# Optimization experiments

Measured on AMD Instinct MI355X. Metric: run time of the kernel, lower is better.

The kernel has to match this reference:

```python
import jax, jax.numpy as jnp
import numpy as np

FEATURE_DIM = 1024
HEADS = 16
HEAD_DIM = FEATURE_DIM // HEADS


def setup_inputs() -> dict:
    key = jax.random.key(0)
    ks = jax.random.split(key, 9)
    B, C, T = 4, FEATURE_DIM, 4096
    s = 1.0 / np.sqrt(C)
    inp = {
        "x": jax.random.normal(ks[0], (B, C, T), dtype=jnp.float32),
        "Wq": jax.random.uniform(ks[1], (C, C), jnp.float32, -s, s),
        "bq": jax.random.uniform(ks[2], (C,), jnp.float32, -s, s),
        "Wk": jax.random.uniform(ks[3], (C, C), jnp.float32, -s, s),
        "bk": jax.random.uniform(ks[4], (C,), jnp.float32, -s, s),
        "Wv": jax.random.uniform(ks[5], (C, C), jnp.float32, -s, s),
        "bv": jax.random.uniform(ks[6], (C,), jnp.float32, -s, s),
        "Wo": jax.random.uniform(ks[7], (C, C), jnp.float32, -s, s),
        "bo": jax.random.uniform(ks[8], (C,), jnp.float32, -s, s),
    }
    return inp


def reference(x, Wq, bq, Wk, bk, Wv, bv, Wo, bo):
    B, C, T = x.shape
    H, D = HEADS, HEAD_DIM
    xt = jnp.transpose(x, (0, 2, 1))  # [B, T, C]
    # torch Linear: y = x @ W.T + b
    q = jax.nn.elu(xt @ Wq.T + bq).reshape(B, T, H, D) + 1.0
    k = jax.nn.elu(xt @ Wk.T + bk).reshape(B, T, H, D) + 1.0
    v = (xt @ Wv.T + bv).reshape(B, T, H, D)
    kv = jnp.einsum('bthd,bthe->bhde', k, v)      # [B, H, D, D]
    z = jnp.einsum('bthd,bhd->bth', q, k.sum(axis=1))  # [B, T, H]
    num = jnp.einsum('bthd,bhde->bthe', q, kv)    # [B, T, H, D]
    out = num / (z[..., None] + 1e-6)
    out = out.reshape(B, T, C)
    out = out @ Wo.T + bo  # dropout is identity in eval mode
    return jnp.transpose(out + xt, (0, 2, 1))  # [B, C, T]
```

## Files before the change

kernel.cpp:

```cpp
#include <hip/hip_runtime.h>
#include <hip/hip_bf16.h>
#include <cmath>

typedef unsigned short u16;
typedef unsigned int   u32;

#define BB 4
#define CC 1024
#define TT 4096
#define HH 16
#define DD 64

using bf16x8 = __attribute__((ext_vector_type(8))) __bf16;
using f32x4  = __attribute__((ext_vector_type(4))) float;

union FragU { bf16x8 v; u16 u[8]; };

__device__ __forceinline__ float bf2f(u16 u) {
    union { u32 i; float f; } v; v.i = ((u32)u) << 16; return v.f;
}
__device__ __forceinline__ u16 f2bf(float f) {
    union { float f; u32 i; } v; v.f = f;
    u32 x = v.i;
    return (u16)((x + 0x7fffu + ((x >> 16) & 1u)) >> 16);
}

__device__ __forceinline__ void gl_lds16(const u16* g, u16* l) {
    __builtin_amdgcn_global_load_lds(
        (const __attribute__((address_space(1))) void*)g,
        (__attribute__((address_space(3))) void*)l, 16, 0, 0);
}

__global__ __launch_bounds__(256) void cvt_kernel(
    const float* __restrict__ src, u16* __restrict__ dst, int n)
{
    const int i = (blockIdx.x * 256 + threadIdx.x) * 4;
    if (i < n) {
        const float4 v = *reinterpret_cast<const float4*>(src + i);
        ushort4 o;
        o.x = f2bf(v.x); o.y = f2bf(v.y); o.z = f2bf(v.z); o.w = f2bf(v.w);
        *reinterpret_cast<ushort4*>(dst + i) = o;
    }
}

__global__ __launch_bounds__(256) void transpose_kernel(
    const float* __restrict__ x, u16* __restrict__ xt)
{
    __shared__ u16 tile[64 * 258];
    const int b  = blockIdx.z;
    const int t0 = blockIdx.x * 64;
    const int c0 = blockIdx.y * 256;
    const float* xb  = x  + (size_t)b * CC * TT;
    u16*         xtb = xt + (size_t)b * TT * CC;

    const int tcol = threadIdx.x & 63;
    const int rw   = threadIdx.x >> 6;
    #pragma unroll 8
    for (int p = 0; p < 64; ++p) {
        const int cr = p * 4 + rw;
        tile[tcol * 258 + cr] = f2bf(xb[(size_t)(c0 + cr) * TT + t0 + tcol]);
    }
    __syncthreads();
    const int cp = threadIdx.x & 127;
    const int th = threadIdx.x >> 7;
    #pragma unroll 8
    for (int q = 0; q < 32; ++q) {
        const int tr = q * 2 + th;
        const u32 v = *reinterpret_cast<const u32*>(&tile[tr * 258 + cp * 2]);
        *reinterpret_cast<u32*>(&xtb[(size_t)(t0 + tr) * CC + c0 + cp * 2]) = v;
    }
}

template <int MODE>
__global__ __launch_bounds__(256, 2) void gemm_kernel(
    const u16* __restrict__ A, const u16* __restrict__ W,
    const float* __restrict__ b0, const float* __restrict__ b1,
    const float* __restrict__ b2, u16* __restrict__ Ybf,
    float* __restrict__ Yf, const float* __restrict__ xres,
    int M, int N, int K)
{
    __shared__ char smem[34048];
    u16* As = (u16*)smem;
    u16* Ws = (u16*)(smem + 16384);

    const int tid  = threadIdx.x;
    const int w    = tid >> 6;
    const int lane = tid & 63;
    const int wm = w >> 1, wn = w & 1;
    const int quad = lane >> 4, l16 = lane & 15;
    const int m0 = blockIdx.y * 128;
    const int n0 = blockIdx.x * 128;

    const int srow = lane >> 3;
    const int scol = ((lane & 7) ^ srow) * 8;

    f32x4 acc[4][4];
    #pragma unroll
    for (int i = 0; i < 4; ++i)
        #pragma unroll
        for (int j = 0; j < 4; ++j) acc[i][j] = (f32x4)0.0f;

    for (int k0 = 0; k0 < K; k0 += 64) {
        __syncthreads();
        #pragma unroll
        for (int s = 0; s < 4; ++s)
            gl_lds16(A + (size_t)(m0 + 32 * w + 8 * s + srow) * K + k0 + scol,
                     &As[(32 * w + 8 * s) * 64]);
        #pragma unroll
        for (int s = 0; s < 4; ++s)
            gl_lds16(W + (size_t)(n0 + 32 * w + 8 * s + srow) * K + k0 + scol,
                     &Ws[(32 * w + 8 * s) * 64]);
        __syncthreads();

        #pragma unroll
        for (int sub = 0; sub < 2; ++sub) {
            const int pg = (((sub << 2) | quad) ^ (l16 & 7)) * 8;
            bf16x8 af[4], bfr[4];
            #pragma unroll
            for (int i = 0; i < 4; ++i) {
                af[i]  = *reinterpret_cast<const bf16x8*>(&As[(wm * 64 + i * 16 + l16) * 64 + pg]);
                bfr[i] = *reinterpret_cast<const bf16x8*>(&Ws[(wn * 64 + i * 16 + l16) * 64 + pg]);
            }
            #pragma unroll
            for (int i = 0; i < 4; ++i)
                #pragma unroll
                for (int j = 0; j < 4; ++j)
                    acc[i][j] = __builtin_amdgcn_mfma_f32_16x16x32_bf16(af[i], bfr[j], acc[i][j], 0, 0, 0);
        }
    }

    if (MODE == 2) {
        float* Cs = (float*)smem;
        const int b     = m0 / TT;
        const int tbase = m0 - b * TT;
        const int cl    = lane >> 4;
        #pragma unroll
        for (int hh = 0; hh < 2; ++hh) {
            __syncthreads();
            if (wm == hh) {
                #pragma unroll
                for (int i = 0; i < 4; ++i)
                    #pragma unroll
                    for (int j = 0; j < 4; ++j)
                        #pragma unroll
                        for (int r = 0; r < 4; ++r)
                            Cs[(i * 16 + quad * 4 + r) * 133 + wn * 64 + j * 16 + l16] = acc[i][j][r];
            }
            __syncthreads();
            #pragma unroll
            for (int p = 0; p < 8; ++p) {
                const int col = p * 16 + w * 4 + cl;
                const int tl  = l16 * 4;
                float4 v;
                v.x = Cs[(tl + 0) * 133 + col];
                v.y = Cs[(tl + 1) * 133 + col];
                v.z = Cs[(tl + 2) * 133 + col];
                v.w = Cs[(tl + 3) * 133 + col];
                const float bv = b0[n0 + col];
                const size_t base = ((size_t)b * CC + n0 + col) * TT + tbase + hh * 64 + tl;
                const float4 rx = *reinterpret_cast<const float4*>(&xres[base]);
                v.x += bv + rx.x; v.y += bv + rx.y;
                v.z += bv + rx.z; v.w += bv + rx.w;
                *reinterpret_cast<float4*>(&Yf[base]) = v;
            }
        }
    } else {
        const int seg = n0 >> 10;
        const float* bp = (seg == 0) ? b0 : ((seg == 1) ? b1 : b2);
        u16* Yseg = Ybf + (size_t)seg * M * CC;
        #pragma unroll
        for (int i = 0; i < 4; ++i) {
            const int row = m0 + wm * 64 + i * 16 + quad * 4;
            #pragma unroll
            for (int j = 0; j < 4; ++j) {
                const int colL = (n0 & 1023) + wn * 64 + j * 16 + l16;
                const float bv = bp[colL];
                #pragma unroll
                for (int r = 0; r < 4; ++r) {
                    float v = acc[i][j][r] + bv;
                    if (seg < 2) v = (v > 0.0f) ? (v + 1.0f) : __expf(v);
                    Yseg[(size_t)(row + r) * CC + colL] = f2bf(v);
                }
            }
        }
    }
}

__global__ __launch_bounds__(256) void kv_kernel(
    const u16* __restrict__ Km, const u16* __restrict__ Vm,
    float* __restrict__ kv, float* __restrict__ ksum)
{
    __shared__ u16 Ks[32 * 64];
    __shared__ u16 Vs[32 * 64];
    const int bh = blockIdx.x;
    const int b = bh >> 4, h = bh & 15;
    const int tc0 = blockIdx.y * 512;
    const int tid = threadIdx.x;
    const int w = tid >> 6, lane = tid & 63;
    const int quad = lane >> 4, l16 = lane & 15;
    const u16* Kbase = Km + (size_t)b * TT * CC + h * DD;
    const u16* Vbase = Vm + (size_t)b * TT * CC + h * DD;

    const int srow = 8 * w + (lane >> 3);
    const int scol = (lane & 7) * 8;

    f32x4 acc[4];
    #pragma unroll
    for (int j = 0; j < 4; ++j) acc[j] = (f32x4)0.0f;
    f32x4 ks = (f32x4)0.0f;

    FragU ones;
    #pragma unroll
    for (int j = 0; j < 8; ++j) ones.u[j] = (l16 == 0) ? 0x3F80u : 0u;

    for (int c = 0; c < 16; ++c) {
        const int t0 = tc0 + 32 * c;
        __syncthreads();
        gl_lds16(Kbase + (size_t)(t0 + srow) * CC + scol, &Ks[8 * w * 64]);
        gl_lds16(Vbase + (size_t)(t0 + srow) * CC + scol, &Vs[8 * w * 64]);
        __syncthreads();

        FragU af;
        #pragma unroll
        for (int j = 0; j < 8; ++j)
            af.u[j] = Ks[(quad * 8 + j) * 64 + w * 16 + l16];
        #pragma unroll
        for (int e4 = 0; e4 < 4; ++e4) {
            FragU bf;
            #pragma unroll
            for (int j = 0; j < 8; ++j)
                bf.u[j] = Vs[(quad * 8 + j) * 64 + e4 * 16 + l16];
            acc[e4] = __builtin_amdgcn_mfma_f32_16x16x32_bf16(af.v, bf.v, acc[e4], 0, 0, 0);
        }
        ks = __builtin_amdgcn_mfma_f32_16x16x32_bf16(af.v, ones.v, ks, 0, 0, 0);
    }

    float* kvb = kv + (size_t)bh * DD * DD;
    #pragma unroll
    for (int e4 = 0; e4 < 4; ++e4)
        #pragma unroll
        for (int r = 0; r < 4; ++r)
            atomicAdd(&kvb[(w * 16 + quad * 4 + r) * DD + e4 * 16 + l16], acc[e4][r]);
    if (l16 == 0) {
        #pragma unroll
        for (int r = 0; r < 4; ++r)
            atomicAdd(&ksum[bh * DD + w * 16 + quad * 4 + r], ks[r]);
    }
}

__global__ __launch_bounds__(256) void attn_kernel(
    const u16* __restrict__ Q, const float* __restrict__ kv,
    const float* __restrict__ ksum, u16* __restrict__ attn)
{
    __shared__ float kvs[DD * DD];
    __shared__ float kss[DD];
    const int bh = blockIdx.x;
    const int b = bh >> 4, h = bh & 15;
    const int tb = blockIdx.y * 256;
    const int tid = threadIdx.x;
    const int w = tid >> 6, lane = tid & 63;
    const int quad = lane >> 4, l16 = lane & 15;

    const float* kvb = kv + (size_t)bh * DD * DD;
    {
        const float4* s4 = reinterpret_cast<const float4*>(kvb);
        float4* d4 = reinterpret_cast<float4*>(kvs);
        #pragma unroll
        for (int p = 0; p < 4; ++p) d4[p * 256 + tid] = s4[p * 256 + tid];
        if (tid < DD) kss[tid] = ksum[bh * DD + tid];
    }
    __syncthreads();

    FragU bf[4][2], zb[2];
    #pragma unroll
    for (int ck = 0; ck < 2; ++ck) {
        #pragma unroll
        for (int nt = 0; nt < 4; ++nt)
            #pragma unroll
            for (int j = 0; j < 8; ++j)
                bf[nt][ck].u[j] = f2bf(kvs[(ck * 32 + quad * 8 + j) * DD + nt * 16 + l16]);
        #pragma unroll
        for (int j = 0; j < 8; ++j)
            zb[ck].u[j] = (l16 == 0) ? f2bf(kss[ck * 32 + quad * 8 + j]) : 0u;
    }

    f32x4 acc[4][4], zacc[4];
    #pragma unroll
    for (int i = 0; i < 4; ++i) {
        zacc[i] = (f32x4)0.0f;
        #pragma unroll
        for (int j = 0; j < 4; ++j) acc[i][j] = (f32x4)0.0f;
    }

    const u16* Qbase = Q + ((size_t)b * TT) * CC + h * DD;
    #pragma unroll
    for (int i = 0; i < 4; ++i) {
        const int t = tb + w * 64 + i * 16 + l16;
        #pragma unroll
        for (int ck = 0; ck < 2; ++ck) {
            const bf16x8 af = *reinterpret_cast<const bf16x8*>(
                Qbase + (size_t)t * CC + ck * 32 + quad * 8);
            #pragma unroll
            for (int nt = 0; nt < 4; ++nt)
                acc[i][nt] = __builtin_amdgcn_mfma_f32_16x16x32_bf16(af, bf[nt][ck].v, acc[i][nt], 0, 0, 0);
            zacc[i] = __builtin_amdgcn_mfma_f32_16x16x32_bf16(af, zb[ck].v, zacc[i], 0, 0, 0);
        }
    }

    u16* obase = attn + ((size_t)b * TT) * CC + h * DD;
    #pragma unroll
    for (int i = 0; i < 4; ++i) {
        float inv[4];
        #pragma unroll
        for (int r = 0; r < 4; ++r) {
            const float zv = __shfl(zacc[i][r], lane & 48);
            inv[r] = 1.0f / (zv + 1e-6f);
        }
        #pragma unroll
        for (int nt = 0; nt < 4; ++nt) {
            #pragma unroll
            for (int r = 0; r < 4; ++r) {
                const int t = tb + w * 64 + i * 16 + quad * 4 + r;
                obase[(size_t)t * CC + nt * 16 + l16] = f2bf(acc[i][nt][r] * inv[r]);
            }
        }
    }
}

extern "C" void kernel_launch(void* const* d_in, const int* in_sizes, int n_in,
                              void* d_out, int out_size, void* d_ws, size_t ws_size,
                              hipStream_t stream)
{
    const float* x  = (const float*)d_in[0];
    const float* Wq = (const float*)d_in[1];
    const float* bq = (const float*)d_in[2];
    const float* Wk = (const float*)d_in[3];
    const float* bk = (const float*)d_in[4];
    const float* Wv = (const float*)d_in[5];
    const float* bv = (const float*)d_in[6];
    const float* Wo = (const float*)d_in[7];
    const float* bo = (const float*)d_in[8];
    float* out = (float*)d_out;

    const int M = BB * TT;
    const size_t BUF  = (size_t)BB * TT * CC * sizeof(u16);
    const size_t WBUF = (size_t)CC * CC * sizeof(u16);

    char* ws = (char*)d_ws;
    u16* xt   = (u16*)(ws);
    u16* Qb   = (u16*)(ws + BUF);
    u16* Wcat = (u16*)(ws + 4 * BUF);
    u16* Wob  = (u16*)(ws + 4 * BUF + 3 * WBUF);
    float* kvbuf = (float*)(ws + 4 * BUF + 4 * WBUF);
    float* ksumb = (float*)(ws + 4 * BUF + 4 * WBUF
                            + (size_t)BB * HH * DD * DD * sizeof(float));
    u16* attn = xt;

    hipMemsetAsync(kvbuf, 0,
        (size_t)(BB * HH * DD * DD + BB * HH * DD) * sizeof(float), stream);

    const int wn = CC * CC;
    cvt_kernel<<<wn / 1024, 256, 0, stream>>>(Wq, Wcat, wn);
    cvt_kernel<<<wn / 1024, 256, 0, stream>>>(Wk, Wcat + (size_t)wn, wn);
    cvt_kernel<<<wn / 1024, 256, 0, stream>>>(Wv, Wcat + 2 * (size_t)wn, wn);
    cvt_kernel<<<wn / 1024, 256, 0, stream>>>(Wo, Wob, wn);

    transpose_kernel<<<dim3(TT / 64, CC / 256, BB), 256, 0, stream>>>(x, xt);

    gemm_kernel<3><<<dim3(3 * CC / 128, M / 128), 256, 0, stream>>>(
        xt, Wcat, bq, bk, bv, Qb, nullptr, nullptr, M, 3 * CC, CC);

    kv_kernel<<<dim3(BB * HH, TT / 512), 256, 0, stream>>>(
        Qb + (size_t)M * CC, Qb + 2 * (size_t)M * CC, kvbuf, ksumb);

    attn_kernel<<<dim3(BB * HH, TT / 256), 256, 0, stream>>>(Qb, kvbuf, ksumb, attn);

    gemm_kernel<2><<<dim3(CC / 128, M / 128), 256, 0, stream>>>(
        attn, Wob, bo, nullptr, nullptr, nullptr, out, x, M, CC, CC);
}
```

Baseline: 358.0 us.

## Store K/V transposed, swizzle LDS tiles, fuse prep launches and zeroing

The QKV GEMM epilogue now writes K and V in a [B, C, T] layout. kv_kernel can then load contiguous time runs per feature and read MFMA fragments with vectorized, XOR-swizzled LDS loads instead of scalar gathers. attn_kernel stages its Q tile into LDS through direct global-to-LDS loads. The four weight conversions, the input transpose and the kv/ksum memset are merged into one prep kernel to cut launch overhead. The trade-off is that the K/V epilogue stores become strided 8-byte writes, and attn_kernel uses more shared memory.

```diff
diff --git a/kernel.cpp b/kernel.cpp
--- a/kernel.cpp
+++ b/kernel.cpp
@@ -31,43 +31,52 @@
         (__attribute__((address_space(3))) void*)l, 16, 0, 0);
 }
 
-__global__ __launch_bounds__(256) void cvt_kernel(
-    const float* __restrict__ src, u16* __restrict__ dst, int n)
+__global__ __launch_bounds__(256) void prep_kernel(
+    const float* __restrict__ x,
+    const float* __restrict__ Wq, const float* __restrict__ Wk,
+    const float* __restrict__ Wv, const float* __restrict__ Wo,
+    u16* __restrict__ xt, u16* __restrict__ Wcat, u16* __restrict__ Wob,
+    float* __restrict__ kvz)
 {
-    const int i = (blockIdx.x * 256 + threadIdx.x) * 4;
-    if (i < n) {
+    __shared__ u16 tile[64 * 258];
+    const int id  = blockIdx.x;
+    const int tid = threadIdx.x;
+
+    if (id < 1024) {
+        const int t0 = (id & 63) * 64;
+        const int c0 = ((id >> 6) & 3) * 256;
+        const int b  = id >> 8;
+        const float* xb  = x  + (size_t)b * CC * TT;
+        u16*         xtb = xt + (size_t)b * TT * CC;
+        const int tcol = tid & 63;
+        const int rw   = tid >> 6;
+        #pragma unroll 8
+        for (int p = 0; p < 64; ++p) {
+            const int cr = p * 4 + rw;
+            tile[tcol * 258 + cr] = f2bf(xb[(size_t)(c0 + cr) * TT + t0 + tcol]);
+        }
+        __syncthreads();
+        const int cp = tid & 127;
+        const int th = tid >> 7;
+        #pragma unroll 8
+        for (int q = 0; q < 32; ++q) {
+            const int tr = q * 2 + th;
+            const u32 v = *reinterpret_cast<const u32*>(&tile[tr * 258 + cp * 2]);
+            *reinterpret_cast<u32*>(&xtb[(size_t)(t0 + tr) * CC + c0 + cp * 2]) = v;
+        }
+    } else if (id < 5120) {
+        const int id2  = id - 1024;
+        const int wsel = id2 >> 10;
+        const int i    = ((id2 & 1023) * 256 + tid) * 4;
+        const float* src = (wsel == 0) ? Wq : (wsel == 1) ? Wk : (wsel == 2) ? Wv : Wo;
+        u16* dst = (wsel < 3) ? (Wcat + (size_t)wsel * CC * CC) : Wob;
         const float4 v = *reinterpret_cast<const float4*>(src + i);
         ushort4 o;
         o.x = f2bf(v.x); o.y = f2bf(v.y); o.z = f2bf(v.z); o.w = f2bf(v.w);
         *reinterpret_cast<ushort4*>(dst + i) = o;
-    }
-}
-
-__global__ __launch_bounds__(256) void transpose_kernel(
-    const float* __restrict__ x, u16* __restrict__ xt)
-{
-    __shared__ u16 tile[64 * 258];
-    const int b  = blockIdx.z;
-    const int t0 = blockIdx.x * 64;
-    const int c0 = blockIdx.y * 256;
-    const float* xb  = x  + (size_t)b * CC * TT;
-    u16*         xtb = xt + (size_t)b * TT * CC;
-
-    const int tcol = threadIdx.x & 63;
-    const int rw   = threadIdx.x >> 6;
-    #pragma unroll 8
-    for (int p = 0; p < 64; ++p) {
-        const int cr = p * 4 + rw;
-        tile[tcol * 258 + cr] = f2bf(xb[(size_t)(c0 + cr) * TT + t0 + tcol]);
-    }
-    __syncthreads();
-    const int cp = threadIdx.x & 127;
-    const int th = threadIdx.x >> 7;
-    #pragma unroll 8
-    for (int q = 0; q < 32; ++q) {
-        const int tr = q * 2 + th;
-        const u32 v = *reinterpret_cast<const u32*>(&tile[tr * 258 + cp * 2]);
-        *reinterpret_cast<u32*>(&xtb[(size_t)(t0 + tr) * CC + c0 + cp * 2]) = v;
+    } else {
+        const int idx = ((id - 5120) * 256 + tid) * 4;
+        *reinterpret_cast<float4*>(&kvz[idx]) = (float4){0.f, 0.f, 0.f, 0.f};
     }
 }
 
@@ -167,42 +176,65 @@
     } else {
         const int seg = n0 >> 10;
         const float* bp = (seg == 0) ? b0 : ((seg == 1) ? b1 : b2);
-        u16* Yseg = Ybf + (size_t)seg * M * CC;
-        #pragma unroll
-        for (int i = 0; i < 4; ++i) {
-            const int row = m0 + wm * 64 + i * 16 + quad * 4;
-            #pragma unroll
-            for (int j = 0; j < 4; ++j) {
-                const int colL = (n0 & 1023) + wn * 64 + j * 16 + l16;
-                const float bv = bp[colL];
+        if (seg == 0) {
+            #pragma unroll
+            for (int i = 0; i < 4; ++i) {
+                const int row = m0 + wm * 64 + i * 16 + quad * 4;
                 #pragma unroll
-                for (int r = 0; r < 4; ++r) {
-                    float v = acc[i][j][r] + bv;
-                    if (seg < 2) v = (v > 0.0f) ? (v + 1.0f) : __expf(v);
-                    Yseg[(size_t)(row + r) * CC + colL] = f2bf(v);
+                for (int j = 0; j < 4; ++j) {
+                    const int colL = wn * 64 + j * 16 + l16;
+                    const float bv = bp[colL];
+                    #pragma unroll
+                    for (int r = 0; r < 4; ++r) {
+                        float v = acc[i][j][r] + bv;
+                        v = (v > 0.0f) ? (v + 1.0f) : __expf(v);
+                        Ybf[(size_t)(row + r) * CC + colL] = f2bf(v);
+                    }
                 }
             }
+        } else {
+            u16* Yt = Ybf + (size_t)seg * M * CC;
+            const int b = m0 / TT;
+            #pragma unroll
+            for (int i = 0; i < 4; ++i) {
+                const int t = (m0 - b * TT) + wm * 64 + i * 16 + quad * 4;
+                #pragma unroll
+                for (int j = 0; j < 4; ++j) {
+                    const int colL = (n0 & 1023) + wn * 64 + j * 16 + l16;
+                    const float bv = bp[colL];
+                    ushort4 o;
+                    #pragma unroll
+                    for (int r = 0; r < 4; ++r) {
+                        float v = acc[i][j][r] + bv;
+                        if (seg == 1) v = (v > 0.0f) ? (v + 1.0f) : __expf(v);
+                        ((u16*)&o)[r] = f2bf(v);
+                    }
+                    *reinterpret_cast<ushort4*>(
+                        &Yt[((size_t)(b * CC + colL)) * TT + t]) = o;
+                }
+            }
         }
     }
 }
 
 __global__ __launch_bounds__(256) void kv_kernel(
-    const u16* __restrict__ Km, const u16* __restrict__ Vm,
+    const u16* __restrict__ Kt, const u16* __restrict__ Vt,
     float* __restrict__ kv, float* __restrict__ ksum)
 {
-    __shared__ u16 Ks[32 * 64];
-    __shared__ u16 Vs[32 * 64];
+    __shared__ u16 Ks[64 * 64];
+    __shared__ u16 Vs[64 * 64];
     const int bh = blockIdx.x;
     const int b = bh >> 4, h = bh & 15;
     const int tc0 = blockIdx.y * 512;
     const int tid = threadIdx.x;
     const int w = tid >> 6, lane = tid & 63;
     const int quad = lane >> 4, l16 = lane & 15;
-    const u16* Kbase = Km + (size_t)b * TT * CC + h * DD;
-    const u16* Vbase = Vm + (size_t)b * TT * CC + h * DD;
-
-    const int srow = 8 * w + (lane >> 3);
-    const int scol = (lane & 7) * 8;
+
+    const u16* Kg = Kt + ((size_t)(b * CC + h * DD)) * TT;
+    const u16* Vg = Vt + ((size_t)(b * CC + h * DD)) * TT;
+
+    const int srow = lane >> 3;
+    const int scol = ((lane & 7) ^ srow) * 8;
 
     f32x4 acc[4];
     #pragma unroll
@@ -213,26 +245,31 @@
     #pragma unroll
     for (int j = 0; j < 8; ++j) ones.u[j] = (l16 == 0) ? 0x3F80u : 0u;
 
-    for (int c = 0; c < 16; ++c) {
-        const int t0 = tc0 + 32 * c;
+    for (int it = 0; it < 8; ++it) {
+        const int t0 = tc0 + it * 64;
         __syncthreads();
-        gl_lds16(Kbase + (size_t)(t0 + srow) * CC + scol, &Ks[8 * w * 64]);
-        gl_lds16(Vbase + (size_t)(t0 + srow) * CC + scol, &Vs[8 * w * 64]);
+        #pragma unroll
+        for (int s = 0; s < 2; ++s) {
+            gl_lds16(Kg + (size_t)(16 * w + 8 * s + srow) * TT + t0 + scol,
+                     &Ks[(16 * w + 8 * s) * 64]);
+            gl_lds16(Vg + (size_t)(16 * w + 8 * s + srow) * TT + t0 + scol,
+                     &Vs[(16 * w + 8 * s) * 64]);
+        }
         __syncthreads();
 
-        FragU af;
-        #pragma unroll
-        for (int j = 0; j < 8; ++j)
-            af.u[j] = Ks[(quad * 8 + j) * 64 + w * 16 + l16];
-        #pragma unroll
-        for (int e4 = 0; e4 < 4; ++e4) {
-            FragU bf;
-            #pragma unroll
-            for (int j = 0; j < 8; ++j)
-                bf.u[j] = Vs[(quad * 8 + j) * 64 + e4 * 16 + l16];
-            acc[e4] = __builtin_amdgcn_mfma_f32_16x16x32_bf16(af.v, bf.v, acc[e4], 0, 0, 0);
-        }
-        ks = __builtin_amdgcn_mfma_f32_16x16x32_bf16(af.v, ones.v, ks, 0, 0, 0);
+        #pragma unroll
+        for (int sub = 0; sub < 2; ++sub) {
+            const int pg = (((sub << 2) | quad) ^ (l16 & 7)) * 8;
+            const bf16x8 af = *reinterpret_cast<const bf16x8*>(
+                &Ks[(w * 16 + l16) * 64 + pg]);
+            #pragma unroll
+            for (int e4 = 0; e4 < 4; ++e4) {
+                const bf16x8 bfv = *reinterpret_cast<const bf16x8*>(
+                    &Vs[(e4 * 16 + l16) * 64 + pg]);
+                acc[e4] = __builtin_amdgcn_mfma_f32_16x16x32_bf16(af, bfv, acc[e4], 0, 0, 0);
+            }
+            ks = __builtin_amdgcn_mfma_f32_16x16x32_bf16(af, ones.v, ks, 0, 0, 0);
+        }
     }
 
     float* kvb = kv + (size_t)bh * DD * DD;
@@ -252,6 +289,7 @@
     const u16* __restrict__ Q, const float* __restrict__ kv,
     const float* __restrict__ ksum, u16* __restrict__ attn)
 {
+    __shared__ u16 Qs[256 * 64];
     __shared__ float kvs[DD * DD];
     __shared__ float kss[DD];
     const int bh = blockIdx.x;
@@ -261,9 +299,17 @@
     const int w = tid >> 6, lane = tid & 63;
     const int quad = lane >> 4, l16 = lane & 15;
 
-    const float* kvb = kv + (size_t)bh * DD * DD;
     {
-        const float4* s4 = reinterpret_cast<const float4*>(kvb);
+        const int srow = lane >> 3;
+        const int scol = ((lane & 7) ^ srow) * 8;
+        const u16* Qg = Q + ((size_t)(b * TT + tb)) * CC + h * DD;
+        #pragma unroll
+        for (int p = 0; p < 8; ++p)
+            gl_lds16(Qg + (size_t)(64 * w + 8 * p + srow) * CC + scol,
+                     &Qs[(64 * w + 8 * p) * 64]);
+    }
+    {
+        const float4* s4 = reinterpret_cast<const float4*>(kv + (size_t)bh * DD * DD);
         float4* d4 = reinterpret_cast<float4*>(kvs);
         #pragma unroll
         for (int p = 0; p < 4; ++p) d4[p * 256 + tid] = s4[p * 256 + tid];
@@ -292,14 +338,13 @@
         for (int j = 0; j < 4; ++j) acc[i][j] = (f32x4)0.0f;
     }
 
-    const u16* Qbase = Q + ((size_t)b * TT) * CC + h * DD;
     #pragma unroll
     for (int i = 0; i < 4; ++i) {
-        const int t = tb + w * 64 + i * 16 + l16;
+        const int trow = w * 64 + i * 16 + l16;
         #pragma unroll
         for (int ck = 0; ck < 2; ++ck) {
-            const bf16x8 af = *reinterpret_cast<const bf16x8*>(
-                Qbase + (size_t)t * CC + ck * 32 + quad * 8);
+            const int pg = (((ck << 2) | quad) ^ (l16 & 7)) * 8;
+            const bf16x8 af = *reinterpret_cast<const bf16x8*>(&Qs[trow * 64 + pg]);
             #pragma unroll
             for (int nt = 0; nt < 4; ++nt)
                 acc[i][nt] = __builtin_amdgcn_mfma_f32_16x16x32_bf16(af, bf[nt][ck].v, acc[i][nt], 0, 0, 0);
@@ -352,20 +397,10 @@
     u16* Wcat = (u16*)(ws + 4 * BUF);
     u16* Wob  = (u16*)(ws + 4 * BUF + 3 * WBUF);
     float* kvbuf = (float*)(ws + 4 * BUF + 4 * WBUF);
-    float* ksumb = (float*)(ws + 4 * BUF + 4 * WBUF
-                            + (size_t)BB * HH * DD * DD * sizeof(float));
+    float* ksumb = kvbuf + (size_t)BB * HH * DD * DD;
     u16* attn = xt;
 
-    hipMemsetAsync(kvbuf, 0,
-        (size_t)(BB * HH * DD * DD + BB * HH * DD) * sizeof(float), stream);
-
-    const int wn = CC * CC;
-    cvt_kernel<<<wn / 1024, 256, 0, stream>>>(Wq, Wcat, wn);
-    cvt_kernel<<<wn / 1024, 256, 0, stream>>>(Wk, Wcat + (size_t)wn, wn);
-    cvt_kernel<<<wn / 1024, 256, 0, stream>>>(Wv, Wcat + 2 * (size_t)wn, wn);
-    cvt_kernel<<<wn / 1024, 256, 0, stream>>>(Wo, Wob, wn);
-
-    transpose_kernel<<<dim3(TT / 64, CC / 256, BB), 256, 0, stream>>>(x, xt);
+    prep_kernel<<<5380, 256, 0, stream>>>(x, Wq, Wk, Wv, Wo, xt, Wcat, Wob, kvbuf);
 
     gemm_kernel<3><<<dim3(3 * CC / 128, M / 128), 256, 0, stream>>>(
         xt, Wcat, bq, bk, bv, Qb, nullptr, nullptr, M, 3 * CC, CC);
```

Result: no change. 352.4 us (-1.6%).
